# Kernel tuning notes

Measured on AMD Instinct MI355X. Metric: run time of the kernel, lower is better.

Reference implementation:

```python
import jax, jax.numpy as jnp
import numpy as np

ITERS = 3
EPS = 1e-10

def _ln(x, g, b):
    m = x.mean(-1, keepdims=True)
    v = ((x - m) ** 2).mean(-1, keepdims=True)
    return (x - m) * jax.lax.rsqrt(v + 1e-5) * g + b

def _gru(x, h, W_ih, W_hh, b_ih, b_hh):
    d = h.shape[-1]
    gi = x @ W_ih.T + b_ih
    gh = h @ W_hh.T + b_hh
    r = jax.nn.sigmoid(gi[:, :d] + gh[:, :d])
    z = jax.nn.sigmoid(gi[:, d:2 * d] + gh[:, d:2 * d])
    nc = jnp.tanh(gi[:, 2 * d:] + r * gh[:, 2 * d:])
    return (1.0 - z) * nc + z * h

def setup_inputs():
    key = jax.random.key(0)
    ks = jax.random.split(key, 16)
    b, n, d, ns, hid = 4, 4096, 128, 16, 512
    s = 0.05
    rn = lambda i, shp: jax.random.normal(ks[i], shp, jnp.float32) * s
    return {
        'slots': jax.random.normal(ks[0], (b, ns, 2 * d), jnp.float32),
        'inputs': jax.random.normal(ks[1], (b, n, d), jnp.float32),
        'Wq': rn(2, (d, d)), 'Wk': rn(3, (d, d)), 'Wv': rn(4, (d, d)),
        'W_ih': rn(5, (3 * d, d)), 'W_hh': rn(6, (3 * d, d)),
        'b_ih': jnp.zeros((3 * d,), jnp.float32), 'b_hh': jnp.zeros((3 * d,), jnp.float32),
        'mu_W1': rn(7, (hid, d)), 'mu_b1': jnp.zeros((hid,), jnp.float32),
        'mu_W2': rn(8, (d, hid)), 'mu_b2': jnp.zeros((d,), jnp.float32),
        'g_in': jnp.ones((d,), jnp.float32), 'be_in': jnp.zeros((d,), jnp.float32),
        'g_sl': jnp.ones((2 * d,), jnp.float32), 'be_sl': jnp.zeros((2 * d,), jnp.float32),
        'g_mu': jnp.ones((d,), jnp.float32), 'be_mu': jnp.zeros((d,), jnp.float32),
        'out_W1': rn(9, (2 * hid, 2 * d)), 'out_b1': jnp.zeros((2 * hid,), jnp.float32),
        'out_W2': rn(10, (d, 2 * hid)), 'out_b2': jnp.zeros((d,), jnp.float32),
    }

def _forward(slots, inputs, Wq, Wk, Wv, W_ih, W_hh, b_ih, b_hh, mu_W1, mu_b1, mu_W2, mu_b2,
             g_in, be_in, g_sl, be_sl, g_mu, be_mu, out_W1, out_b1, out_W2, out_b2):
    b, n, d = inputs.shape
    ns = slots.shape[1]
    scale = d ** -0.5
    x = _ln(inputs, g_in, be_in)
    k = x @ Wk.T
    v = x @ Wv.T
    pi_cl = jnp.ones((b, ns, 1), inputs.dtype) / ns

    def step(slots, pi_cl):
        sl = _ln(slots, g_sl, be_sl)
        mu, logsig = sl[..., :d], sl[..., d:]
        q_mu = mu @ Wq.T
        q_ls = logsig @ Wq.T
        inv_var = jnp.exp(-2.0 * q_ls)  # 1 / exp(q_logsigma)^2
        diff = k[:, None, :, :] - q_mu[:, :, None, :]  # (b, ns, n, d)
        dots = (diff ** 2 * inv_var[:, :, None, :]).sum(-1) * scale  # (b, ns, n)
        dots_exp = (jnp.exp(-dots) + EPS) * pi_cl
        attn = dots_exp / dots_exp.sum(1, keepdims=True)   # normalize over slots
        attn = attn / attn.sum(-1, keepdims=True)          # normalize over tokens
        upd = jnp.einsum('bjd,bij->bid', v, attn)
        pi_new = attn.sum(-1, keepdims=True)
        pi_new = pi_new / (pi_new.sum(1, keepdims=True) + EPS)
        upd = _gru(upd.reshape(-1, d), mu.reshape(-1, d), W_ih, W_hh, b_ih, b_hh).reshape(b, ns, d)
        h = _ln(upd, g_mu, be_mu)
        upd = upd + (jax.nn.relu(h @ mu_W1.T + mu_b1) @ mu_W2.T + mu_b2)
        diff_v = v[:, None, :, :] - upd[:, :, None, :]  # (b, ns, n, d)
        ls = 0.5 * jnp.log(jnp.einsum('bijd,bij->bid', diff_v ** 2 + EPS, attn))
        return jnp.concatenate([upd, ls], axis=-1), pi_new, attn

    for _ in range(ITERS):
        slots, pi_cl, attn = step(slots, pi_cl)
    slots, pi_cl, attn = step(jax.lax.stop_gradient(slots), pi_cl)
    slots_out = jax.nn.relu(slots @ out_W1.T + out_b1) @ out_W2.T + out_b2
    return slots_out, attn

def reference(slots, inputs, Wq, Wk, Wv, W_ih, W_hh, b_ih, b_hh, mu_W1, mu_b1, mu_W2, mu_b2,
              g_in, be_in, g_sl, be_sl, g_mu, be_mu, out_W1, out_b1, out_W2, out_b2):
    return _forward(slots, inputs, Wq, Wk, Wv, W_ih, W_hh, b_ih, b_hh, mu_W1, mu_b1, mu_W2, mu_b2,
                    g_in, be_in, g_sl, be_sl, g_mu, be_mu, out_W1, out_b1, out_W2, out_b2)
```

## Files before the change

### kernel.cpp

```cpp
#include <hip/hip_runtime.h>
#include <math.h>

#define B_ 4
#define N_ 4096
#define D_ 128
#define NS_ 16
#define NT_ 64
#define SCALE_ 0.08838834764831843f
#define EPS_ 1e-10f

#define OFF_K      ((size_t)0)
#define OFF_V      (OFF_K + (size_t)B_*N_*D_)
#define OFF_WTKV   (OFF_V + (size_t)B_*N_*D_)
#define OFF_WCP    (OFF_WTKV + 128*256)
#define OFF_M1P    (OFF_WCP + 128*512)
#define OFF_M2P    (OFF_M1P + 64*512)
#define OFF_WQP    (OFF_M2P + 256*128)
#define OFF_O1P    (OFF_WQP + 64*128)
#define OFF_O2P    (OFF_O1P + 128*1024)
#define OFF_MU     (OFF_O2P + 512*128)
#define OFF_WCOEF  (OFF_MU + (size_t)B_*NS_*128)
#define OFF_C      (OFF_WCOEF + (size_t)B_*128*32)
#define OFF_PART   (OFF_C + 64)
#define OFF_ATTNU  (OFF_PART + (size_t)B_*NT_*NS_*260)

#define S_ZS    0
#define S_S2    256
#define S_UU    384
#define S_H2    512
#define S_A1S   640
#define S_SNEW  1152
#define S_QM    1408
#define S_QL    1536
#define S_RED   1664
#define S_P1    2688
#define S_TOT   3712

__device__ __forceinline__ float bf_lo(unsigned p) { return __uint_as_float(p << 16); }
__device__ __forceinline__ float bf_hi(unsigned p) { return __uint_as_float(p & 0xffff0000u); }
__device__ __forceinline__ unsigned packbf(float lo, float hi) {
  unsigned ul = __float_as_uint(lo), uh = __float_as_uint(hi);
  ul = (ul + 0x7fffu + ((ul >> 16) & 1u)) >> 16;
  uh = (uh + 0x7fffu + ((uh >> 16) & 1u)) >> 16;
  return (ul & 0xffffu) | (uh << 16);
}

__device__ __forceinline__ float waveRed1(float a) {
  #pragma unroll
  for (int off = 32; off > 0; off >>= 1) a += __shfl_down(a, off, 64);
  return a;
}
__device__ __forceinline__ float2 waveRed2(float a, float b) {
  #pragma unroll
  for (int off = 32; off > 0; off >>= 1) {
    a += __shfl_down(a, off, 64);
    b += __shfl_down(b, off, 64);
  }
  return make_float2(a, b);
}

struct SW {
  const unsigned* wcP;
  const unsigned* m1P;
  const unsigned* m2P;
  const unsigned* wqP;
  const float* bih; const float* bhh;
  const float* mb1; const float* mb2;
  const float* gmu; const float* bmu;
  const float* gsl; const float* bsl;
};

__device__ __forceinline__ void slotTail1024(float* sl, int b, int i, int tid,
    const unsigned* __restrict__ wqPu, float* wcoef, float* cbuf) {
  float* red = sl + S_RED;
  {
    int rest = tid & 255, kg = tid >> 8;
    int wh = rest >> 7, o = rest & 127;
    const uint2* wq = (const uint2*)wqPu + (size_t)(kg * 8) * 128 + o;
    const float* s = sl + S_A1S + wh * 128 + kg * 32;
    float a0 = 0.f, a1 = 0.f, a2 = 0.f, a3 = 0.f;
    #pragma unroll
    for (int r = 0; r < 8; ++r) {
      uint2 p = wq[r * 128];
      a0 = fmaf(s[4 * r],     bf_lo(p.x), a0);
      a1 = fmaf(s[4 * r + 1], bf_hi(p.x), a1);
      a2 = fmaf(s[4 * r + 2], bf_lo(p.y), a2);
      a3 = fmaf(s[4 * r + 3], bf_hi(p.y), a3);
    }
    sl[S_P1 + kg * 256 + rest] = (a0 + a1) + (a2 + a3);
  }
  __syncthreads();
  if (tid < 256) {
    float q = sl[S_P1 + tid] + sl[S_P1 + 256 + tid] + sl[S_P1 + 512 + tid] + sl[S_P1 + 768 + tid];
    if (tid < 128) sl[S_QM + tid] = q; else sl[S_QL + (tid - 128)] = q;
  }
  __syncthreads();
  if (tid < 128) {
    float iv = expf(-2.f * sl[S_QL + tid]);
    float a1 = SCALE_ * iv;
    float a2 = -2.f * SCALE_ * iv * sl[S_QM + tid];
    float* wrow = &wcoef[(((size_t)b * 16 + i) * 128 + tid) * 2];
    wrow[0] = a2;
    wrow[1] = a1;
    float cp = SCALE_ * iv * sl[S_QM + tid] * sl[S_QM + tid];
    float r = waveRed1(cp);
    if ((tid & 63) == 0) red[16 + (tid >> 6)] = r;
  }
  __syncthreads();
  if (tid == 0) cbuf[b * NS_ + i] = red[16] + red[17];
}

template <int FINAL>
__device__ void slotUpdateT(float* sl, int b, int i, int tid,
    const float* __restrict__ part, float* mu, float* wcoef, float* cbuf, SW w) {
  float* red = sl + S_RED;
  size_t pbase = ((size_t)(b * NT_) * NS_ + i) * 260;
  const size_t pstr = (size_t)NS_ * 260;
  {
    int g = tid >> 8, e = tid & 255;
    float s = 0.f;
    #pragma unroll 16
    for (int t = 0; t < 16; ++t) s += part[pbase + (size_t)(g * 16 + t) * pstr + e];
    sl[S_P1 + g * 256 + e] = s;
  }
  if (tid < 64) {
    float rtv = waveRed1(part[pbase + (size_t)tid * pstr + 256]);
    if (tid == 0) red[0] = rtv;
  }
  __syncthreads();
  float rt = red[0];
  if (tid < 256) {
    float s = sl[S_P1 + tid] + sl[S_P1 + 256 + tid] + sl[S_P1 + 512 + tid] + sl[S_P1 + 768 + tid];
    if (tid < 128) sl[S_ZS + tid] = s / rt; else sl[S_S2 + tid - 128] = s / rt;
  } else if (tid < 384) {
    sl[S_ZS + tid - 128] = mu[(size_t)(b * NS_ + i) * 128 + (tid - 256)];
  }
  __syncthreads();
  {
    int q = tid & 511, kg = tid >> 9;
    const uint2* wcol = (const uint2*)w.wcP + (size_t)(kg * 32) * 512 + q;
    const float* xz = sl + S_ZS + kg * 128;
    float a0 = 0.f, a1 = 0.f, a2 = 0.f, a3 = 0.f;
    #pragma unroll 16
    for (int r = 0; r < 32; ++r) {
      uint2 p = wcol[r * 512];
      a0 = fmaf(xz[4 * r],     bf_lo(p.x), a0);
      a1 = fmaf(xz[4 * r + 1], bf_hi(p.x), a1);
      a2 = fmaf(xz[4 * r + 2], bf_lo(p.y), a2);
      a3 = fmaf(xz[4 * r + 3], bf_hi(p.y), a3);
    }
    sl[S_P1 + kg * 512 + q] = (a0 + a1) + (a2 + a3);
  }
  __syncthreads();
  float uu_reg = 0.f;
  if (tid < 128) {
    float o_r = sl[S_P1 + tid] + sl[S_P1 + 512 + tid];
    float o_z = sl[S_P1 + 128 + tid] + sl[S_P1 + 640 + tid];
    float o_n = sl[S_P1 + 256 + tid] + sl[S_P1 + 768 + tid];
    float o_g = sl[S_P1 + 384 + tid] + sl[S_P1 + 896 + tid];
    float r = 1.f / (1.f + expf(-(o_r + w.bih[tid] + w.bhh[tid])));
    float z = 1.f / (1.f + expf(-(o_z + w.bih[128 + tid] + w.bhh[128 + tid])));
    float nn = tanhf(o_n + w.bih[256 + tid] + r * (o_g + w.bhh[256 + tid]));
    uu_reg = (1.f - z) * nn + z * sl[S_ZS + 128 + tid];
    sl[S_UU + tid] = uu_reg;
    float2 r2 = waveRed2(uu_reg, uu_reg * uu_reg);
    if ((tid & 63) == 0) { red[4 + (tid >> 6) * 2] = r2.x; red[5 + (tid >> 6) * 2] = r2.y; }
  }
  __syncthreads();
  if (tid < 128) {
    float sum = red[4] + red[6], sq = red[5] + red[7];
    float m = sum * (1.f / 128.f);
    float var = sq * (1.f / 128.f) - m * m;
    float rsq = rsqrtf(var + 1e-5f);
    sl[S_H2 + tid] = (uu_reg - m) * rsq * w.gmu[tid] + w.bmu[tid];
  }
  __syncthreads();
  {
    int q = tid & 511, kg = tid >> 9;
    const uint2* wc1 = (const uint2*)w.m1P + (size_t)(kg * 16) * 512 + q;
    const float* h = sl + S_H2 + kg * 64;
    float a0 = 0.f, a1 = 0.f, a2 = 0.f, a3 = 0.f;
    #pragma unroll
    for (int r = 0; r < 16; ++r) {
      uint2 p = wc1[r * 512];
      a0 = fmaf(h[4 * r],     bf_lo(p.x), a0);
      a1 = fmaf(h[4 * r + 1], bf_hi(p.x), a1);
      a2 = fmaf(h[4 * r + 2], bf_lo(p.y), a2);
      a3 = fmaf(h[4 * r + 3], bf_hi(p.y), a3);
    }
    sl[S_P1 + kg * 512 + q] = (a0 + a1) + (a2 + a3);
  }
  __syncthreads();
  if (tid < 512)
    sl[S_A1S + tid] = fmaxf(sl[S_P1 + tid] + sl[S_P1 + 512 + tid] + w.mb1[tid], 0.f);
  __syncthreads();
  {
    int d = tid & 127, qg = tid >> 7;
    const uint2* wc2 = (const uint2*)w.m2P + (size_t)(qg * 16) * 128 + d;
    const float* a = sl + S_A1S + qg * 64;
    float b0 = 0.f, b1 = 0.f, b2 = 0.f, b3 = 0.f;
    #pragma unroll
    for (int r = 0; r < 16; ++r) {
      uint2 p = wc2[r * 128];
      b0 = fmaf(a[4 * r],     bf_lo(p.x), b0);
      b1 = fmaf(a[4 * r + 1], bf_hi(p.x), b1);
      b2 = fmaf(a[4 * r + 2], bf_lo(p.y), b2);
      b3 = fmaf(a[4 * r + 3], bf_hi(p.y), b3);
    }
    sl[S_P1 + qg * 128 + d] = (b0 + b1) + (b2 + b3);
  }
  __syncthreads();
  if (tid < 128) {
    float o = w.mb2[tid];
    #pragma unroll
    for (int g = 0; g < 8; ++g) o += sl[S_P1 + g * 128 + tid];
    float uf = sl[S_UU + tid] + o;
    float xsv = sl[S_ZS + tid];
    float arg = sl[S_S2 + tid] - 2.f * uf * xsv + uf * uf + EPS_;
    float lsv = 0.5f * logf(fmaxf(arg, 1e-30f));
    sl[S_SNEW + tid] = uf;
    sl[S_SNEW + 128 + tid] = lsv;
  }
  __syncthreads();
  if (FINAL) return;
  float xv = 0.f;
  if (tid < 256) {
    xv = sl[S_SNEW + tid];
    float2 r2 = waveRed2(xv, xv * xv);
    if ((tid & 63) == 0) { red[8 + (tid >> 6) * 2] = r2.x; red[9 + (tid >> 6) * 2] = r2.y; }
  }
  __syncthreads();
  if (tid < 256) {
    float sum = red[8] + red[10] + red[12] + red[14];
    float sq = red[9] + red[11] + red[13] + red[15];
    float m2 = sum * (1.f / 256.f);
    float var2 = sq * (1.f / 256.f) - m2 * m2;
    float rs2 = rsqrtf(var2 + 1e-5f);
    float slv = (xv - m2) * rs2 * w.gsl[tid] + w.bsl[tid];
    sl[S_A1S + tid] = slv;
    if (tid < 128) mu[(size_t)(b * NS_ + i) * 128 + tid] = slv;
  }
  __syncthreads();
  slotTail1024(sl, b, i, tid, w.wqP, wcoef, cbuf);
}

__global__ __launch_bounds__(256) void tK(
    const float* __restrict__ Wq, const float* __restrict__ Wk, const float* __restrict__ Wv,
    const float* __restrict__ Wih, const float* __restrict__ Whh,
    const float* __restrict__ mW1, const float* __restrict__ mW2,
    float* __restrict__ ws) {
  int tid = blockIdx.x * blockDim.x + threadIdx.x;
  int stride = gridDim.x * blockDim.x;
  uint2* wcP = (uint2*)(ws + OFF_WCP);
  uint2* m1P = (uint2*)(ws + OFF_M1P);
  uint2* m2P = (uint2*)(ws + OFF_M2P);
  uint2* wqP = (uint2*)(ws + OFF_WQP);
  for (int idx = tid; idx < 128 * 256; idx += stride) {
    int kk = idx >> 8, c = idx & 255;
    ws[OFF_WTKV + idx] = (c < 128) ? Wk[c * 128 + kk] : Wv[(c - 128) * 128 + kk];
  }
  for (int idx = tid; idx < 64 * 512; idx += stride) {
    int r2 = idx >> 9, q = idx & 511;
    float v[4];
    #pragma unroll
    for (int j = 0; j < 4; ++j) {
      int dd = 4 * r2 + j;
      float val;
      if (dd < 128) {
        val = (q < 384) ? Wih[q * 128 + dd] : 0.f;
      } else {
        int dh = dd - 128;
        if (q < 256)      val = Whh[q * 128 + dh];
        else if (q < 384) val = 0.f;
        else              val = Whh[(q - 128) * 128 + dh];
      }
      v[j] = val;
    }
    wcP[idx] = make_uint2(packbf(v[0], v[1]), packbf(v[2], v[3]));
  }
  for (int idx = tid; idx < 32 * 512; idx += stride) {
    int r2 = idx >> 9, q = idx & 511;
    m1P[idx] = make_uint2(packbf(mW1[q * 128 + 4 * r2], mW1[q * 128 + 4 * r2 + 1]),
                          packbf(mW1[q * 128 + 4 * r2 + 2], mW1[q * 128 + 4 * r2 + 3]));
  }
  for (int idx = tid; idx < 128 * 128; idx += stride) {
    int qq = idx >> 7, d = idx & 127;
    m2P[idx] = make_uint2(packbf(mW2[d * 512 + 4 * qq], mW2[d * 512 + 4 * qq + 1]),
                          packbf(mW2[d * 512 + 4 * qq + 2], mW2[d * 512 + 4 * qq + 3]));
  }
  for (int idx = tid; idx < 32 * 128; idx += stride) {
    int r2 = idx >> 7, o = idx & 127;
    wqP[idx] = make_uint2(packbf(Wq[o * 128 + 4 * r2], Wq[o * 128 + 4 * r2 + 1]),
                          packbf(Wq[o * 128 + 4 * r2 + 2], Wq[o * 128 + 4 * r2 + 3]));
  }
}

__global__ __launch_bounds__(1024, 1) void kvK(const float* __restrict__ inp,
    const float* __restrict__ wt, const float* __restrict__ gin, const float* __restrict__ bin,
    const float* __restrict__ slots_in, SW w,
    const float* __restrict__ oW1, const float* __restrict__ oW2,
    unsigned* __restrict__ o1P, unsigned* __restrict__ o2P,
    float* __restrict__ kb, float* __restrict__ vb,
    float* __restrict__ mu, float* wcoef, float* cbuf) {
  __shared__ __align__(16) float shm[9600];
  int tid = threadIdx.x;
  int blk = blockIdx.x;
  if (blk < 256) {
    float* xs = shm;
    float* red = shm + 8448;
    float* mrow = shm + 9472;
    float* rrow = shm + 9536;
    int rowbase = blk * 64;
    #pragma unroll
    for (int it = 0; it < 2; ++it) {
      int f = tid + it * 1024;
      int row = f >> 5, c4 = (f & 31) * 4;
      const float4 v = *(const float4*)&inp[(size_t)(rowbase + row) * 128 + c4];
      *(float4*)&xs[row * 132 + c4] = v;
    }
    __syncthreads();
    int row = tid >> 4, prt = tid & 15;
    float s = 0.f, s2 = 0.f;
    #pragma unroll
    for (int e = 0; e < 8; ++e) {
      float v = xs[row * 132 + prt * 8 + e];
      s += v; s2 = fmaf(v, v, s2);
    }
    red[row * 16 + prt] = s;
    __syncthreads();
    if (prt == 0) {
      float m = 0.f;
      #pragma unroll
      for (int q = 0; q < 16; ++q) m += red[row * 16 + q];
      mrow[row] = m * (1.f / 128.f);
    }
    __syncthreads();
    float m = mrow[row];
    red[row * 16 + prt] = s2;
    __syncthreads();
    if (prt == 0) {
      float v = 0.f;
      #pragma unroll
      for (int q = 0; q < 16; ++q) v += red[row * 16 + q];
      float var = v * (1.f / 128.f) - m * m;
      rrow[row] = rsqrtf(var + 1e-5f);
    }
    __syncthreads();
    float rs = rrow[row];
    #pragma unroll
    for (int e = 0; e < 8; ++e) {
      int c = prt * 8 + e;
      xs[row * 132 + c] = (xs[row * 132 + c] - m) * rs * gin[c] + bin[c];
    }
    __syncthreads();
    int l = tid & 63;
    int wv = __builtin_amdgcn_readfirstlane(threadIdx.x >> 6);
    int cbase = wv * 16;
    float acc[16];
    #pragma unroll
    for (int e = 0; e < 16; ++e) acc[e] = 0.f;
    #pragma unroll 4
    for (int kk = 0; kk < 128; kk += 2) {
      float2 xv = *(const float2*)&xs[l * 132 + kk];
      const float* wr0 = &wt[kk * 256 + cbase];
      const float* wr1 = &wt[(kk + 1) * 256 + cbase];
      #pragma unroll
      for (int e = 0; e < 16; ++e) {
        acc[e] = fmaf(xv.x, wr0[e], acc[e]);
        acc[e] = fmaf(xv.y, wr1[e], acc[e]);
      }
    }
    float* outp = (cbase < 128) ? kb : vb;
    int col = cbase & 127;
    size_t o = (size_t)(rowbase + l) * 128 + col;
    #pragma unroll
    for (int e4 = 0; e4 < 4; ++e4)
      *(float4*)&outp[o + e4 * 4] =
          make_float4(acc[e4 * 4], acc[e4 * 4 + 1], acc[e4 * 4 + 2], acc[e4 * 4 + 3]);
  } else if (blk < 320) {
    float* sl = shm;
    float* red = sl + S_RED;
    int sb = blk - 256;
    int b2 = sb >> 4, i = sb & 15;
    float xv = 0.f;
    if (tid < 256) {
      xv = slots_in[(size_t)(b2 * NS_ + i) * 256 + tid];
      float2 r2 = waveRed2(xv, xv * xv);
      if ((tid & 63) == 0) { red[8 + (tid >> 6) * 2] = r2.x; red[9 + (tid >> 6) * 2] = r2.y; }
    }
    __syncthreads();
    if (tid < 256) {
      float sum = red[8] + red[10] + red[12] + red[14];
      float sq = red[9] + red[11] + red[13] + red[15];
      float m = sum * (1.f / 256.f);
      float var = sq * (1.f / 256.f) - m * m;
      float rs = rsqrtf(var + 1e-5f);
      float slv = (xv - m) * rs * w.gsl[tid] + w.bsl[tid];
      sl[S_A1S + tid] = slv;
      if (tid < 128) mu[(size_t)(b2 * NS_ + i) * 128 + tid] = slv;
    }
    __syncthreads();
    slotTail1024(sl, b2, i, tid, w.wqP, wcoef, cbuf);
  } else {
    int pb = blk - 320;
    uint2* o1 = (uint2*)o1P;
    {
      int idx = pb * 1024 + tid;
      int r2 = idx >> 10, q = idx & 1023;
      o1[idx] = make_uint2(packbf(oW1[q * 256 + 4 * r2], oW1[q * 256 + 4 * r2 + 1]),
                           packbf(oW1[q * 256 + 4 * r2 + 2], oW1[q * 256 + 4 * r2 + 3]));
    }
    if (pb < 32) {
      uint2* o2 = (uint2*)o2P;
      int idx = pb * 1024 + tid;
      int qq = idx >> 7, d = idx & 127;
      o2[idx] = make_uint2(packbf(oW2[d * 1024 + 4 * qq], oW2[d * 1024 + 4 * qq + 1]),
                           packbf(oW2[d * 1024 + 4 * qq + 2], oW2[d * 1024 + 4 * qq + 3]));
    }
  }
}

__global__ __launch_bounds__(1024, 1) void pK(const float* __restrict__ kb,
    const float* __restrict__ vb, const float* __restrict__ wcoef,
    const float* __restrict__ cbuf, float* __restrict__ part,
    float* __restrict__ attnu, int last) {
  __shared__ __align__(16) float buf[64 * 132];
  __shared__ __align__(16) float a1s[16 * 68];
  __shared__ float esum[16 * 64];
  int tid = threadIdx.x;
  int jt = blockIdx.x, b = blockIdx.y;
  size_t jrow = (size_t)(b * N_ + jt * 64);
  #pragma unroll
  for (int it = 0; it < 2; ++it) {
    int f = tid + it * 1024;
    int row = f >> 5, c4 = (f & 31) * 4;
    float4 kv = *(const float4*)&kb[(jrow + row) * 128 + c4];
    *(float4*)&buf[row * 132 + c4] = kv;
  }
  __syncthreads();
  float4 vr0, vr1;
  {
    int f0 = tid, f1 = tid + 1024;
    vr0 = *(const float4*)&vb[(jrow + (f0 >> 5)) * 128 + (f0 & 31) * 4];
    vr1 = *(const float4*)&vb[(jrow + (f1 >> 5)) * 128 + (f1 & 31) * 4];
  }
  {
    int l = tid & 63;
    int w = __builtin_amdgcn_readfirstlane(threadIdx.x >> 6);
    const float* wq = &wcoef[((size_t)b * 16 + w) * 256];
    float c0 = cbuf[b * NS_ + w];
    float a0 = 0.f, a1 = 0.f, a2 = 0.f, a3 = 0.f;
    #pragma unroll 8
    for (int kk = 0; kk < 128; kk += 4) {
      float4 kv = *(const float4*)&buf[l * 132 + kk];
      float4 wA = *(const float4*)&wq[kk * 2];
      float4 wB = *(const float4*)&wq[kk * 2 + 4];
      a0 = fmaf(fmaf(wA.y, kv.x, wA.x), kv.x, a0);
      a1 = fmaf(fmaf(wA.w, kv.y, wA.z), kv.y, a1);
      a2 = fmaf(fmaf(wB.y, kv.z, wB.x), kv.z, a2);
      a3 = fmaf(fmaf(wB.w, kv.w, wB.z), kv.w, a3);
    }
    float e0 = expf(-(c0 + (a0 + a1) + (a2 + a3))) + EPS_;
    esum[w * 64 + l] = e0;
    __syncthreads();
    float tot = 0.f;
    #pragma unroll
    for (int q = 0; q < 16; ++q) tot += esum[q * 64 + l];
    float av = e0 / tot;
    a1s[w * 68 + l] = av;
    if (last) attnu[(size_t)(b * NS_ + w) * N_ + jt * 64 + l] = av;
  }
  __syncthreads();
  {
    int f0 = tid, f1 = tid + 1024;
    *(float4*)&buf[(f0 >> 5) * 132 + (f0 & 31) * 4] = vr0;
    *(float4*)&buf[(f1 >> 5) * 132 + (f1 & 31) * 4] = vr1;
  }
  __syncthreads();
  {
    int ii = __builtin_amdgcn_readfirstlane(threadIdx.x >> 6);
    int lh = (tid >> 5) & 1;
    int l4 = (tid & 31) * 4;
    float av0 = 0, av1 = 0, av2 = 0, av3 = 0, aw0 = 0, aw1 = 0, aw2 = 0, aw3 = 0, rsum = 0;
    #pragma unroll
    for (int jj = 0; jj < 32; jj += 4) {
      int j = lh * 32 + jj;
      float4 a4 = *(const float4*)&a1s[ii * 68 + j];
      float aarr[4] = {a4.x, a4.y, a4.z, a4.w};
      #pragma unroll
      for (int e = 0; e < 4; ++e) {
        float a = aarr[e];
        float4 v = *(const float4*)&buf[(j + e) * 132 + l4];
        rsum += a;
        float m0 = a * v.x, m1 = a * v.y, m2 = a * v.z, m3 = a * v.w;
        av0 += m0; av1 += m1; av2 += m2; av3 += m3;
        aw0 = fmaf(m0, v.x, aw0); aw1 = fmaf(m1, v.y, aw1);
        aw2 = fmaf(m2, v.z, aw2); aw3 = fmaf(m3, v.w, aw3);
      }
    }
    av0 += __shfl_down(av0, 32, 64); av1 += __shfl_down(av1, 32, 64);
    av2 += __shfl_down(av2, 32, 64); av3 += __shfl_down(av3, 32, 64);
    aw0 += __shfl_down(aw0, 32, 64); aw1 += __shfl_down(aw1, 32, 64);
    aw2 += __shfl_down(aw2, 32, 64); aw3 += __shfl_down(aw3, 32, 64);
    rsum += __shfl_down(rsum, 32, 64);
    if ((tid & 63) < 32) {
      float* pr = &part[((size_t)(b * NT_ + jt) * NS_ + ii) * 260];
      *(float4*)&pr[l4] = make_float4(av0, av1, av2, av3);
      *(float4*)&pr[128 + l4] = make_float4(aw0, aw1, aw2, aw3);
      if ((tid & 63) == 0) pr[256] = rsum;
    }
  }
}

__global__ __launch_bounds__(1024, 1) void rK(const float* __restrict__ part,
    float* mu, float* wcoef, float* cbuf, SW w) {
  __shared__ __align__(16) float sl[S_TOT];
  int tid = threadIdx.x;
  int b = blockIdx.x >> 4, i = blockIdx.x & 15;
  slotUpdateT<0>(sl, b, i, tid, part, mu, wcoef, cbuf, w);
}

__global__ __launch_bounds__(1024, 1) void oK(const float* __restrict__ part,
    float* mu, SW w,
    const unsigned* __restrict__ o1P, const float* __restrict__ ob1,
    const unsigned* __restrict__ o2P, const float* __restrict__ ob2,
    const float* __restrict__ attnu, float* __restrict__ out) {
  __shared__ __align__(16) float sl[S_TOT];
  int blk = blockIdx.x, tid = threadIdx.x;
  const size_t pstr = (size_t)NS_ * 260;
  if (blk >= 64) {
    int r = blk - 64;
    int b = r >> 4, i = r & 15;
    size_t pbase = ((size_t)(b * NT_) * NS_ + i) * 260;
    if (tid < 64) {
      float v = waveRed1(part[pbase + (size_t)tid * pstr + 256]);
      if (tid == 0) sl[0] = v;
    }
    __syncthreads();
    float rs = sl[0];
    int base = r * 4096 + tid * 4;
    float4 v = *(const float4*)&attnu[base];
    v.x /= rs; v.y /= rs; v.z /= rs; v.w /= rs;
    *(float4*)&out[8192 + base] = v;
    return;
  }
  int b = blk >> 4, i = blk & 15;
  slotUpdateT<1>(sl, b, i, tid, part, mu, (float*)nullptr, (float*)nullptr, w);
  {
    const float* sn = sl + S_SNEW;
    const uint2* o1 = (const uint2*)o1P;
    float a0 = 0.f, a1 = 0.f;
    #pragma unroll 8
    for (int r = 0; r < 32; ++r) {
      uint2 p0 = o1[r * 1024 + tid];
      uint2 p1 = o1[(32 + r) * 1024 + tid];
      a0 = fmaf(sn[4 * r],     bf_lo(p0.x), a0);
      a0 = fmaf(sn[4 * r + 1], bf_hi(p0.x), a0);
      a0 = fmaf(sn[4 * r + 2], bf_lo(p0.y), a0);
      a0 = fmaf(sn[4 * r + 3], bf_hi(p0.y), a0);
      a1 = fmaf(sn[128 + 4 * r],     bf_lo(p1.x), a1);
      a1 = fmaf(sn[128 + 4 * r + 1], bf_hi(p1.x), a1);
      a1 = fmaf(sn[128 + 4 * r + 2], bf_lo(p1.y), a1);
      a1 = fmaf(sn[128 + 4 * r + 3], bf_hi(p1.y), a1);
    }
    sl[S_P1 + tid] = fmaxf(a0 + a1 + ob1[tid], 0.f);
  }
  __syncthreads();
  float dpart = 0.f;
  {
    int d = tid & 127, qg = tid >> 7;
    const uint2* wc2 = (const uint2*)o2P + (size_t)(qg * 32) * 128 + d;
    const float* h = sl + S_P1 + qg * 128;
    float b0 = 0.f, b1 = 0.f, b2 = 0.f, b3 = 0.f;
    #pragma unroll 8
    for (int r = 0; r < 32; ++r) {
      uint2 p = wc2[r * 128];
      b0 = fmaf(h[4 * r],     bf_lo(p.x), b0);
      b1 = fmaf(h[4 * r + 1], bf_hi(p.x), b1);
      b2 = fmaf(h[4 * r + 2], bf_lo(p.y), b2);
      b3 = fmaf(h[4 * r + 3], bf_hi(p.y), b3);
    }
    dpart = (b0 + b1) + (b2 + b3);
  }
  __syncthreads();
  {
    int d = tid & 127, qg = tid >> 7;
    sl[qg * 128 + d] = dpart;
  }
  __syncthreads();
  if (tid < 128) {
    float o = ob2[tid];
    #pragma unroll
    for (int g = 0; g < 8; ++g) o += sl[g * 128 + tid];
    out[(size_t)blk * 128 + tid] = o;
  }
}

extern "C" void kernel_launch(void* const* d_in, const int* in_sizes, int n_in,
                              void* d_out, int out_size, void* d_ws, size_t ws_size,
                              hipStream_t stream) {
  const float* slots_in = (const float*)d_in[0];
  const float* inputs   = (const float*)d_in[1];
  const float* Wq  = (const float*)d_in[2];
  const float* Wk  = (const float*)d_in[3];
  const float* Wv  = (const float*)d_in[4];
  const float* Wih = (const float*)d_in[5];
  const float* Whh = (const float*)d_in[6];
  const float* bih = (const float*)d_in[7];
  const float* bhh = (const float*)d_in[8];
  const float* mW1 = (const float*)d_in[9];
  const float* mb1 = (const float*)d_in[10];
  const float* mW2 = (const float*)d_in[11];
  const float* mb2 = (const float*)d_in[12];
  const float* g_in  = (const float*)d_in[13];
  const float* be_in = (const float*)d_in[14];
  const float* g_sl  = (const float*)d_in[15];
  const float* be_sl = (const float*)d_in[16];
  const float* g_mu  = (const float*)d_in[17];
  const float* be_mu = (const float*)d_in[18];
  const float* oW1 = (const float*)d_in[19];
  const float* ob1 = (const float*)d_in[20];
  const float* oW2 = (const float*)d_in[21];
  const float* ob2 = (const float*)d_in[22];
  float* ws  = (float*)d_ws;
  float* out = (float*)d_out;
  (void)in_sizes; (void)n_in; (void)out_size; (void)ws_size;

  SW w;
  w.wcP = (const unsigned*)(ws + OFF_WCP);
  w.m1P = (const unsigned*)(ws + OFF_M1P);
  w.m2P = (const unsigned*)(ws + OFF_M2P);
  w.wqP = (const unsigned*)(ws + OFF_WQP);
  w.bih = bih; w.bhh = bhh; w.mb1 = mb1; w.mb2 = mb2;
  w.gmu = g_mu; w.bmu = be_mu; w.gsl = g_sl; w.bsl = be_sl;

  hipLaunchKernelGGL(tK, dim3(64), dim3(256), 0, stream,
                     Wq, Wk, Wv, Wih, Whh, mW1, mW2, ws);
  hipLaunchKernelGGL(kvK, dim3(384), dim3(1024), 0, stream,
                     inputs, ws + OFF_WTKV, g_in, be_in, slots_in, w,
                     oW1, oW2, (unsigned*)(ws + OFF_O1P), (unsigned*)(ws + OFF_O2P),
                     ws + OFF_K, ws + OFF_V, ws + OFF_MU, ws + OFF_WCOEF, ws + OFF_C);
  for (int s = 0; s < 4; ++s) {
    hipLaunchKernelGGL(pK, dim3(64, 4), dim3(1024), 0, stream,
                       ws + OFF_K, ws + OFF_V, ws + OFF_WCOEF, ws + OFF_C,
                       ws + OFF_PART, ws + OFF_ATTNU, (s == 3) ? 1 : 0);
    if (s < 3) {
      hipLaunchKernelGGL(rK, dim3(64), dim3(1024), 0, stream,
                         ws + OFF_PART, ws + OFF_MU, ws + OFF_WCOEF, ws + OFF_C, w);
    }
  }
  hipLaunchKernelGGL(oK, dim3(128), dim3(1024), 0, stream,
                     ws + OFF_PART, ws + OFF_MU, w,
                     (const unsigned*)(ws + OFF_O1P), ob1,
                     (const unsigned*)(ws + OFF_O2P), ob2, ws + OFF_ATTNU, out);
}
```

Measured before the change: 143.7 us.

## Store K/V in bf16 and fold weight-packing kernel into kvK

K and V projections are now written as packed bf16 instead of fp32, halving the buffers that the attention kernel pK rereads on each of its four launches and shrinking its shared-memory tile. The separate weight-transpose and packing kernel tK is removed. Its packing work moves into the spare blocks of kvK, and the K/V projection and initial slot tail read the original fp32 weights directly. This cuts one launch and the traffic on the hot attention loop, at the cost of bf16 rounding of K and V, which affects the distance and variance sums.

```diff
diff --git a/kernel.cpp b/kernel.cpp
--- a/kernel.cpp
+++ b/kernel.cpp
@@ -10,15 +10,14 @@
 #define EPS_ 1e-10f
 
 #define OFF_K      ((size_t)0)
-#define OFF_V      (OFF_K + (size_t)B_*N_*D_)
-#define OFF_WTKV   (OFF_V + (size_t)B_*N_*D_)
-#define OFF_WCP    (OFF_WTKV + 128*256)
-#define OFF_M1P    (OFF_WCP + 128*512)
-#define OFF_M2P    (OFF_M1P + 64*512)
-#define OFF_WQP    (OFF_M2P + 256*128)
-#define OFF_O1P    (OFF_WQP + 64*128)
-#define OFF_O2P    (OFF_O1P + 128*1024)
-#define OFF_MU     (OFF_O2P + 512*128)
+#define OFF_V      (OFF_K + (size_t)B_*N_*64)
+#define OFF_WCP    (OFF_V + (size_t)B_*N_*64)
+#define OFF_M1P    (OFF_WCP + 64*512*2)
+#define OFF_M2P    (OFF_M1P + 32*512*2)
+#define OFF_WQP    (OFF_M2P + 128*128*2)
+#define OFF_O1P    (OFF_WQP + 32*128*2)
+#define OFF_O2P    (OFF_O1P + (size_t)64*1024*2)
+#define OFF_MU     (OFF_O2P + 256*128*2)
 #define OFF_WCOEF  (OFF_MU + (size_t)B_*NS_*128)
 #define OFF_C      (OFF_WCOEF + (size_t)B_*128*32)
 #define OFF_PART   (OFF_C + 64)
@@ -69,27 +68,16 @@
   const float* gmu; const float* bmu;
   const float* gsl; const float* bsl;
 };
-
-__device__ __forceinline__ void slotTail1024(float* sl, int b, int i, int tid,
-    const unsigned* __restrict__ wqPu, float* wcoef, float* cbuf) {
+struct RW {
+  const float* Wq; const float* Wk; const float* Wv;
+  const float* Wih; const float* Whh;
+  const float* mW1; const float* mW2;
+  const float* oW1; const float* oW2;
+};
+
+__device__ __forceinline__ void tailMerge(float* sl, int b, int i, int tid,
+    float* wcoef, float* cbuf) {
   float* red = sl + S_RED;
-  {
-    int rest = tid & 255, kg = tid >> 8;
-    int wh = rest >> 7, o = rest & 127;
-    const uint2* wq = (const uint2*)wqPu + (size_t)(kg * 8) * 128 + o;
-    const float* s = sl + S_A1S + wh * 128 + kg * 32;
-    float a0 = 0.f, a1 = 0.f, a2 = 0.f, a3 = 0.f;
-    #pragma unroll
-    for (int r = 0; r < 8; ++r) {
-      uint2 p = wq[r * 128];
-      a0 = fmaf(s[4 * r],     bf_lo(p.x), a0);
-      a1 = fmaf(s[4 * r + 1], bf_hi(p.x), a1);
-      a2 = fmaf(s[4 * r + 2], bf_lo(p.y), a2);
-      a3 = fmaf(s[4 * r + 3], bf_hi(p.y), a3);
-    }
-    sl[S_P1 + kg * 256 + rest] = (a0 + a1) + (a2 + a3);
-  }
-  __syncthreads();
   if (tid < 256) {
     float q = sl[S_P1 + tid] + sl[S_P1 + 256 + tid] + sl[S_P1 + 512 + tid] + sl[S_P1 + 768 + tid];
     if (tid < 128) sl[S_QM + tid] = q; else sl[S_QL + (tid - 128)] = q;
@@ -108,6 +96,50 @@
   }
   __syncthreads();
   if (tid == 0) cbuf[b * NS_ + i] = red[16] + red[17];
+}
+
+__device__ __forceinline__ void slotTail1024(float* sl, int b, int i, int tid,
+    const unsigned* __restrict__ wqPu, float* wcoef, float* cbuf) {
+  {
+    int rest = tid & 255, kg = tid >> 8;
+    int wh = rest >> 7, o = rest & 127;
+    const uint2* wq = (const uint2*)wqPu + (size_t)(kg * 8) * 128 + o;
+    const float* s = sl + S_A1S + wh * 128 + kg * 32;
+    float a0 = 0.f, a1 = 0.f, a2 = 0.f, a3 = 0.f;
+    #pragma unroll
+    for (int r = 0; r < 8; ++r) {
+      uint2 p = wq[r * 128];
+      a0 = fmaf(s[4 * r],     bf_lo(p.x), a0);
+      a1 = fmaf(s[4 * r + 1], bf_hi(p.x), a1);
+      a2 = fmaf(s[4 * r + 2], bf_lo(p.y), a2);
+      a3 = fmaf(s[4 * r + 3], bf_hi(p.y), a3);
+    }
+    sl[S_P1 + kg * 256 + rest] = (a0 + a1) + (a2 + a3);
+  }
+  __syncthreads();
+  tailMerge(sl, b, i, tid, wcoef, cbuf);
+}
+
+__device__ __forceinline__ void slotTailF(float* sl, int b, int i, int tid,
+    const float* __restrict__ Wq, float* wcoef, float* cbuf) {
+  {
+    int rest = tid & 255, kg = tid >> 8;
+    int wh = rest >> 7, o = rest & 127;
+    const float4* wr = (const float4*)&Wq[(size_t)o * 128 + kg * 32];
+    const float* s = sl + S_A1S + wh * 128 + kg * 32;
+    float a0 = 0.f, a1 = 0.f, a2 = 0.f, a3 = 0.f;
+    #pragma unroll
+    for (int r = 0; r < 8; ++r) {
+      float4 wv = wr[r];
+      a0 = fmaf(s[4 * r],     wv.x, a0);
+      a1 = fmaf(s[4 * r + 1], wv.y, a1);
+      a2 = fmaf(s[4 * r + 2], wv.z, a2);
+      a3 = fmaf(s[4 * r + 3], wv.w, a3);
+    }
+    sl[S_P1 + kg * 256 + rest] = (a0 + a1) + (a2 + a3);
+  }
+  __syncthreads();
+  tailMerge(sl, b, i, tid, wcoef, cbuf);
 }
 
 template <int FINAL>
@@ -244,64 +276,11 @@
   slotTail1024(sl, b, i, tid, w.wqP, wcoef, cbuf);
 }
 
-__global__ __launch_bounds__(256) void tK(
-    const float* __restrict__ Wq, const float* __restrict__ Wk, const float* __restrict__ Wv,
-    const float* __restrict__ Wih, const float* __restrict__ Whh,
-    const float* __restrict__ mW1, const float* __restrict__ mW2,
-    float* __restrict__ ws) {
-  int tid = blockIdx.x * blockDim.x + threadIdx.x;
-  int stride = gridDim.x * blockDim.x;
-  uint2* wcP = (uint2*)(ws + OFF_WCP);
-  uint2* m1P = (uint2*)(ws + OFF_M1P);
-  uint2* m2P = (uint2*)(ws + OFF_M2P);
-  uint2* wqP = (uint2*)(ws + OFF_WQP);
-  for (int idx = tid; idx < 128 * 256; idx += stride) {
-    int kk = idx >> 8, c = idx & 255;
-    ws[OFF_WTKV + idx] = (c < 128) ? Wk[c * 128 + kk] : Wv[(c - 128) * 128 + kk];
-  }
-  for (int idx = tid; idx < 64 * 512; idx += stride) {
-    int r2 = idx >> 9, q = idx & 511;
-    float v[4];
-    #pragma unroll
-    for (int j = 0; j < 4; ++j) {
-      int dd = 4 * r2 + j;
-      float val;
-      if (dd < 128) {
-        val = (q < 384) ? Wih[q * 128 + dd] : 0.f;
-      } else {
-        int dh = dd - 128;
-        if (q < 256)      val = Whh[q * 128 + dh];
-        else if (q < 384) val = 0.f;
-        else              val = Whh[(q - 128) * 128 + dh];
-      }
-      v[j] = val;
-    }
-    wcP[idx] = make_uint2(packbf(v[0], v[1]), packbf(v[2], v[3]));
-  }
-  for (int idx = tid; idx < 32 * 512; idx += stride) {
-    int r2 = idx >> 9, q = idx & 511;
-    m1P[idx] = make_uint2(packbf(mW1[q * 128 + 4 * r2], mW1[q * 128 + 4 * r2 + 1]),
-                          packbf(mW1[q * 128 + 4 * r2 + 2], mW1[q * 128 + 4 * r2 + 3]));
-  }
-  for (int idx = tid; idx < 128 * 128; idx += stride) {
-    int qq = idx >> 7, d = idx & 127;
-    m2P[idx] = make_uint2(packbf(mW2[d * 512 + 4 * qq], mW2[d * 512 + 4 * qq + 1]),
-                          packbf(mW2[d * 512 + 4 * qq + 2], mW2[d * 512 + 4 * qq + 3]));
-  }
-  for (int idx = tid; idx < 32 * 128; idx += stride) {
-    int r2 = idx >> 7, o = idx & 127;
-    wqP[idx] = make_uint2(packbf(Wq[o * 128 + 4 * r2], Wq[o * 128 + 4 * r2 + 1]),
-                          packbf(Wq[o * 128 + 4 * r2 + 2], Wq[o * 128 + 4 * r2 + 3]));
-  }
-}
-
 __global__ __launch_bounds__(1024, 1) void kvK(const float* __restrict__ inp,
-    const float* __restrict__ wt, const float* __restrict__ gin, const float* __restrict__ bin,
-    const float* __restrict__ slots_in, SW w,
-    const float* __restrict__ oW1, const float* __restrict__ oW2,
-    unsigned* __restrict__ o1P, unsigned* __restrict__ o2P,
-    float* __restrict__ kb, float* __restrict__ vb,
-    float* __restrict__ mu, float* wcoef, float* cbuf) {
+    const float* __restrict__ gin, const float* __restrict__ bin,
+    const float* __restrict__ slots_in, SW w, RW rw,
+    unsigned* __restrict__ kb, unsigned* __restrict__ vb,
+    float* __restrict__ mu, float* wcoef, float* cbuf, float* __restrict__ ws) {
   __shared__ __align__(16) float shm[9600];
   int tid = threadIdx.x;
   int blk = blockIdx.x;
@@ -356,27 +335,32 @@
     int l = tid & 63;
     int wv = __builtin_amdgcn_readfirstlane(threadIdx.x >> 6);
     int cbase = wv * 16;
+    const float* wmat = (cbase < 128) ? rw.Wk : rw.Wv;
+    int rowb = cbase & 127;
     float acc[16];
     #pragma unroll
     for (int e = 0; e < 16; ++e) acc[e] = 0.f;
     #pragma unroll 4
-    for (int kk = 0; kk < 128; kk += 2) {
-      float2 xv = *(const float2*)&xs[l * 132 + kk];
-      const float* wr0 = &wt[kk * 256 + cbase];
-      const float* wr1 = &wt[(kk + 1) * 256 + cbase];
+    for (int kk = 0; kk < 128; kk += 4) {
+      float4 xv = *(const float4*)&xs[l * 132 + kk];
       #pragma unroll
       for (int e = 0; e < 16; ++e) {
-        acc[e] = fmaf(xv.x, wr0[e], acc[e]);
-        acc[e] = fmaf(xv.y, wr1[e], acc[e]);
+        const float* wr = &wmat[(size_t)(rowb + e) * 128 + kk];
+        float a = acc[e];
+        a = fmaf(xv.x, wr[0], a);
+        a = fmaf(xv.y, wr[1], a);
+        a = fmaf(xv.z, wr[2], a);
+        a = fmaf(xv.w, wr[3], a);
+        acc[e] = a;
       }
     }
-    float* outp = (cbase < 128) ? kb : vb;
-    int col = cbase & 127;
-    size_t o = (size_t)(rowbase + l) * 128 + col;
-    #pragma unroll
-    for (int e4 = 0; e4 < 4; ++e4)
-      *(float4*)&outp[o + e4 * 4] =
-          make_float4(acc[e4 * 4], acc[e4 * 4 + 1], acc[e4 * 4 + 2], acc[e4 * 4 + 3]);
+    unsigned* outp = (cbase < 128) ? kb : vb;
+    size_t o = (size_t)(rowbase + l) * 64 + (rowb >> 1);
+    unsigned po[8];
+    #pragma unroll
+    for (int e2 = 0; e2 < 8; ++e2) po[e2] = packbf(acc[2 * e2], acc[2 * e2 + 1]);
+    *(uint4*)&outp[o] = make_uint4(po[0], po[1], po[2], po[3]);
+    *(uint4*)&outp[o + 4] = make_uint4(po[4], po[5], po[6], po[7]);
   } else if (blk < 320) {
     float* sl = shm;
     float* red = sl + S_RED;
@@ -400,65 +384,106 @@
       if (tid < 128) mu[(size_t)(b2 * NS_ + i) * 128 + tid] = slv;
     }
     __syncthreads();
-    slotTail1024(sl, b2, i, tid, w.wqP, wcoef, cbuf);
+    slotTailF(sl, b2, i, tid, rw.Wq, wcoef, cbuf);
   } else {
-    int pb = blk - 320;
-    uint2* o1 = (uint2*)o1P;
+    int gid = (blk - 320) * 1024 + tid;
+    uint2* wcP = (uint2*)(ws + OFF_WCP);
+    uint2* m1P = (uint2*)(ws + OFF_M1P);
+    uint2* m2P = (uint2*)(ws + OFF_M2P);
+    uint2* wqP = (uint2*)(ws + OFF_WQP);
+    uint2* o1P = (uint2*)(ws + OFF_O1P);
+    uint2* o2P = (uint2*)(ws + OFF_O2P);
     {
-      int idx = pb * 1024 + tid;
-      int r2 = idx >> 10, q = idx & 1023;
-      o1[idx] = make_uint2(packbf(oW1[q * 256 + 4 * r2], oW1[q * 256 + 4 * r2 + 1]),
-                           packbf(oW1[q * 256 + 4 * r2 + 2], oW1[q * 256 + 4 * r2 + 3]));
-    }
-    if (pb < 32) {
-      uint2* o2 = (uint2*)o2P;
-      int idx = pb * 1024 + tid;
-      int qq = idx >> 7, d = idx & 127;
-      o2[idx] = make_uint2(packbf(oW2[d * 1024 + 4 * qq], oW2[d * 1024 + 4 * qq + 1]),
-                           packbf(oW2[d * 1024 + 4 * qq + 2], oW2[d * 1024 + 4 * qq + 3]));
-    }
-  }
-}
-
-__global__ __launch_bounds__(1024, 1) void pK(const float* __restrict__ kb,
-    const float* __restrict__ vb, const float* __restrict__ wcoef,
+      int r2 = gid >> 10, q = gid & 1023;
+      o1P[gid] = make_uint2(packbf(rw.oW1[q * 256 + 4 * r2], rw.oW1[q * 256 + 4 * r2 + 1]),
+                            packbf(rw.oW1[q * 256 + 4 * r2 + 2], rw.oW1[q * 256 + 4 * r2 + 3]));
+    }
+    if (gid < 32768) {
+      int qq = gid >> 7, d = gid & 127;
+      o2P[gid] = make_uint2(packbf(rw.oW2[d * 1024 + 4 * qq], rw.oW2[d * 1024 + 4 * qq + 1]),
+                            packbf(rw.oW2[d * 1024 + 4 * qq + 2], rw.oW2[d * 1024 + 4 * qq + 3]));
+    }
+    if (gid < 32768) {
+      int r2 = gid >> 9, q = gid & 511;
+      float v[4];
+      #pragma unroll
+      for (int j = 0; j < 4; ++j) {
+        int dd = 4 * r2 + j;
+        float val;
+        if (dd < 128) {
+          val = (q < 384) ? rw.Wih[q * 128 + dd] : 0.f;
+        } else {
+          int dh = dd - 128;
+          if (q < 256)      val = rw.Whh[q * 128 + dh];
+          else if (q < 384) val = 0.f;
+          else              val = rw.Whh[(q - 128) * 128 + dh];
+        }
+        v[j] = val;
+      }
+      wcP[gid] = make_uint2(packbf(v[0], v[1]), packbf(v[2], v[3]));
+    }
+    if (gid < 16384) {
+      int r2 = gid >> 9, q = gid & 511;
+      m1P[gid] = make_uint2(packbf(rw.mW1[q * 128 + 4 * r2], rw.mW1[q * 128 + 4 * r2 + 1]),
+                            packbf(rw.mW1[q * 128 + 4 * r2 + 2], rw.mW1[q * 128 + 4 * r2 + 3]));
+    }
+    if (gid < 16384) {
+      int qq = gid >> 7, d = gid & 127;
+      m2P[gid] = make_uint2(packbf(rw.mW2[d * 512 + 4 * qq], rw.mW2[d * 512 + 4 * qq + 1]),
+                            packbf(rw.mW2[d * 512 + 4 * qq + 2], rw.mW2[d * 512 + 4 * qq + 3]));
+    }
+    if (gid < 4096) {
+      int r2 = gid >> 7, o = gid & 127;
+      wqP[gid] = make_uint2(packbf(rw.Wq[o * 128 + 4 * r2], rw.Wq[o * 128 + 4 * r2 + 1]),
+                            packbf(rw.Wq[o * 128 + 4 * r2 + 2], rw.Wq[o * 128 + 4 * r2 + 3]));
+    }
+  }
+}
+
+__global__ __launch_bounds__(1024, 1) void pK(const unsigned* __restrict__ kb,
+    const unsigned* __restrict__ vb, const float* __restrict__ wcoef,
     const float* __restrict__ cbuf, float* __restrict__ part,
     float* __restrict__ attnu, int last) {
-  __shared__ __align__(16) float buf[64 * 132];
+  __shared__ __align__(16) unsigned buf[64 * 68];
   __shared__ __align__(16) float a1s[16 * 68];
   __shared__ float esum[16 * 64];
   int tid = threadIdx.x;
   int jt = blockIdx.x, b = blockIdx.y;
   size_t jrow = (size_t)(b * N_ + jt * 64);
-  #pragma unroll
-  for (int it = 0; it < 2; ++it) {
-    int f = tid + it * 1024;
-    int row = f >> 5, c4 = (f & 31) * 4;
-    float4 kv = *(const float4*)&kb[(jrow + row) * 128 + c4];
-    *(float4*)&buf[row * 132 + c4] = kv;
-  }
-  __syncthreads();
-  float4 vr0, vr1;
-  {
-    int f0 = tid, f1 = tid + 1024;
-    vr0 = *(const float4*)&vb[(jrow + (f0 >> 5)) * 128 + (f0 & 31) * 4];
-    vr1 = *(const float4*)&vb[(jrow + (f1 >> 5)) * 128 + (f1 & 31) * 4];
+  {
+    int row = tid >> 4, oct = tid & 15;
+    uint4 kv = *(const uint4*)&kb[(jrow + row) * 64 + oct * 4];
+    *(uint4*)&buf[row * 68 + oct * 4] = kv;
+  }
+  __syncthreads();
+  uint4 vr;
+  {
+    int row = tid >> 4, oct = tid & 15;
+    vr = *(const uint4*)&vb[(jrow + row) * 64 + oct * 4];
   }
   {
     int l = tid & 63;
     int w = __builtin_amdgcn_readfirstlane(threadIdx.x >> 6);
-    const float* wq = &wcoef[((size_t)b * 16 + w) * 256];
+    const float4* wq4 = (const float4*)&wcoef[((size_t)b * 16 + w) * 256];
     float c0 = cbuf[b * NS_ + w];
+    const uint4* kr = (const uint4*)&buf[l * 68];
     float a0 = 0.f, a1 = 0.f, a2 = 0.f, a3 = 0.f;
     #pragma unroll 8
-    for (int kk = 0; kk < 128; kk += 4) {
-      float4 kv = *(const float4*)&buf[l * 132 + kk];
-      float4 wA = *(const float4*)&wq[kk * 2];
-      float4 wB = *(const float4*)&wq[kk * 2 + 4];
-      a0 = fmaf(fmaf(wA.y, kv.x, wA.x), kv.x, a0);
-      a1 = fmaf(fmaf(wA.w, kv.y, wA.z), kv.y, a1);
-      a2 = fmaf(fmaf(wB.y, kv.z, wB.x), kv.z, a2);
-      a3 = fmaf(fmaf(wB.w, kv.w, wB.z), kv.w, a3);
+    for (int i = 0; i < 16; ++i) {
+      uint4 kv = kr[i];
+      float4 wA = wq4[4 * i], wB = wq4[4 * i + 1], wC = wq4[4 * i + 2], wD = wq4[4 * i + 3];
+      float k0 = bf_lo(kv.x), k1 = bf_hi(kv.x);
+      float k2 = bf_lo(kv.y), k3 = bf_hi(kv.y);
+      float k4 = bf_lo(kv.z), k5 = bf_hi(kv.z);
+      float k6 = bf_lo(kv.w), k7 = bf_hi(kv.w);
+      a0 = fmaf(fmaf(wA.y, k0, wA.x), k0, a0);
+      a1 = fmaf(fmaf(wA.w, k1, wA.z), k1, a1);
+      a2 = fmaf(fmaf(wB.y, k2, wB.x), k2, a2);
+      a3 = fmaf(fmaf(wB.w, k3, wB.z), k3, a3);
+      a0 = fmaf(fmaf(wC.y, k4, wC.x), k4, a0);
+      a1 = fmaf(fmaf(wC.w, k5, wC.z), k5, a1);
+      a2 = fmaf(fmaf(wD.y, k6, wD.x), k6, a2);
+      a3 = fmaf(fmaf(wD.w, k7, wD.z), k7, a3);
     }
     float e0 = expf(-(c0 + (a0 + a1) + (a2 + a3))) + EPS_;
     esum[w * 64 + l] = e0;
@@ -472,15 +497,14 @@
   }
   __syncthreads();
   {
-    int f0 = tid, f1 = tid + 1024;
-    *(float4*)&buf[(f0 >> 5) * 132 + (f0 & 31) * 4] = vr0;
-    *(float4*)&buf[(f1 >> 5) * 132 + (f1 & 31) * 4] = vr1;
+    int row = tid >> 4, oct = tid & 15;
+    *(uint4*)&buf[row * 68 + oct * 4] = vr;
   }
   __syncthreads();
   {
     int ii = __builtin_amdgcn_readfirstlane(threadIdx.x >> 6);
     int lh = (tid >> 5) & 1;
-    int l4 = (tid & 31) * 4;
+    int dp = tid & 31;
     float av0 = 0, av1 = 0, av2 = 0, av3 = 0, aw0 = 0, aw1 = 0, aw2 = 0, aw3 = 0, rsum = 0;
     #pragma unroll
     for (int jj = 0; jj < 32; jj += 4) {
@@ -490,12 +514,13 @@
       #pragma unroll
       for (int e = 0; e < 4; ++e) {
         float a = aarr[e];
-        float4 v = *(const float4*)&buf[(j + e) * 132 + l4];
+        uint2 q = *(const uint2*)&buf[(j + e) * 68 + dp * 2];
+        float v0 = bf_lo(q.x), v1 = bf_hi(q.x), v2 = bf_lo(q.y), v3 = bf_hi(q.y);
         rsum += a;
-        float m0 = a * v.x, m1 = a * v.y, m2 = a * v.z, m3 = a * v.w;
+        float m0 = a * v0, m1 = a * v1, m2 = a * v2, m3 = a * v3;
         av0 += m0; av1 += m1; av2 += m2; av3 += m3;
-        aw0 = fmaf(m0, v.x, aw0); aw1 = fmaf(m1, v.y, aw1);
-        aw2 = fmaf(m2, v.z, aw2); aw3 = fmaf(m3, v.w, aw3);
+        aw0 = fmaf(m0, v0, aw0); aw1 = fmaf(m1, v1, aw1);
+        aw2 = fmaf(m2, v2, aw2); aw3 = fmaf(m3, v3, aw3);
       }
     }
     av0 += __shfl_down(av0, 32, 64); av1 += __shfl_down(av1, 32, 64);
@@ -505,8 +530,8 @@
     rsum += __shfl_down(rsum, 32, 64);
     if ((tid & 63) < 32) {
       float* pr = &part[((size_t)(b * NT_ + jt) * NS_ + ii) * 260];
-      *(float4*)&pr[l4] = make_float4(av0, av1, av2, av3);
-      *(float4*)&pr[128 + l4] = make_float4(aw0, aw1, aw2, aw3);
+      *(float4*)&pr[dp * 4] = make_float4(av0, av1, av2, av3);
+      *(float4*)&pr[128 + dp * 4] = make_float4(aw0, aw1, aw2, aw3);
       if ((tid & 63) == 0) pr[256] = rsum;
     }
   }
@@ -633,16 +658,18 @@
   w.wqP = (const unsigned*)(ws + OFF_WQP);
   w.bih = bih; w.bhh = bhh; w.mb1 = mb1; w.mb2 = mb2;
   w.gmu = g_mu; w.bmu = be_mu; w.gsl = g_sl; w.bsl = be_sl;
-
-  hipLaunchKernelGGL(tK, dim3(64), dim3(256), 0, stream,
-                     Wq, Wk, Wv, Wih, Whh, mW1, mW2, ws);
+  RW rw;
+  rw.Wq = Wq; rw.Wk = Wk; rw.Wv = Wv; rw.Wih = Wih; rw.Whh = Whh;
+  rw.mW1 = mW1; rw.mW2 = mW2; rw.oW1 = oW1; rw.oW2 = oW2;
+
   hipLaunchKernelGGL(kvK, dim3(384), dim3(1024), 0, stream,
-                     inputs, ws + OFF_WTKV, g_in, be_in, slots_in, w,
-                     oW1, oW2, (unsigned*)(ws + OFF_O1P), (unsigned*)(ws + OFF_O2P),
-                     ws + OFF_K, ws + OFF_V, ws + OFF_MU, ws + OFF_WCOEF, ws + OFF_C);
+                     inputs, g_in, be_in, slots_in, w, rw,
+                     (unsigned*)(ws + OFF_K), (unsigned*)(ws + OFF_V),
+                     ws + OFF_MU, ws + OFF_WCOEF, ws + OFF_C, ws);
   for (int s = 0; s < 4; ++s) {
     hipLaunchKernelGGL(pK, dim3(64, 4), dim3(1024), 0, stream,
-                       ws + OFF_K, ws + OFF_V, ws + OFF_WCOEF, ws + OFF_C,
+                       (const unsigned*)(ws + OFF_K), (const unsigned*)(ws + OFF_V),
+                       ws + OFF_WCOEF, ws + OFF_C,
                        ws + OFF_PART, ws + OFF_ATTNU, (s == 3) ? 1 : 0);
     if (s < 3) {
       hipLaunchKernelGGL(rK, dim3(64), dim3(1024), 0, stream,
```

Result: slower. 185.2 us (+28.9%).
